# Kernel tuning notes

Hardware: AMD Instinct MI355X
Metric: run time of the kernel (lower is better)

Reference implementation:

```python
import jax, jax.numpy as jnp
import numpy as np

N = 100000   # nodes
E = 1600000  # edges
IN, H, OUT = 128, 128, 64
EPS = 1e-5   # BatchNorm1d eps


def setup_inputs() -> dict:
    key = jax.random.key(0)
    ks = jax.random.split(key, 6)
    glorot = lambda k, i, o: jax.random.normal(k, (i, o), jnp.float32) / np.float32(np.sqrt(i))
    return {
        "x": jax.random.normal(ks[0], (N, IN), jnp.float32),
        "edge_index": jax.random.randint(ks[1], (2, E), 0, N, dtype=jnp.int32),
        "W1": glorot(ks[2], IN, H),
        "b1": jnp.zeros((H,), jnp.float32),
        "g1": jnp.ones((H,), jnp.float32),
        "be1": jnp.zeros((H,), jnp.float32),
        "W2": glorot(ks[3], H, H),
        "b2": jnp.zeros((H,), jnp.float32),
        "g2": jnp.ones((H,), jnp.float32),
        "be2": jnp.zeros((H,), jnp.float32),
        "W3": glorot(ks[4], H, OUT),
        "b3": jnp.zeros((OUT,), jnp.float32),
    }


def _gcn_conv(x, W, b, src, dst, dinv):
    # PyG GCNConv: h = x @ W (no linear bias); symmetric-normalized scatter-add
    # over edges with implicit self-loops; then additive bias.
    h = x @ W                                           # [N, F]
    coef = (dinv[src] * dinv[dst])[:, None]             # [E, 1]
    agg = jax.ops.segment_sum(h[src] * coef, dst, num_segments=N)
    agg = agg + h * (dinv * dinv)[:, None]              # self-loop term
    return agg + b


def _bn(x, g, b):
    # BatchNorm1d, training-mode batch statistics (biased variance).
    m = jnp.mean(x, axis=0)
    v = jnp.mean(jnp.square(x - m), axis=0)
    return (x - m) * jax.lax.rsqrt(v + EPS) * g + b


def reference(x, edge_index, W1, b1, g1, be1, W2, b2, g2, be2, W3, b3):
    src, dst = edge_index[0], edge_index[1]
    # degree with self-loops (edge weights = 1)
    deg = jax.ops.segment_sum(jnp.ones((E,), jnp.float32), dst, num_segments=N) + 1.0
    dinv = jax.lax.rsqrt(deg)

    x1 = jax.nn.relu(_bn(_gcn_conv(x, W1, b1, src, dst, dinv), g1, be1))
    x2 = jax.nn.relu(_bn(_gcn_conv(x1, W2, b2, src, dst, dinv), g2, be2))
    x2 = x2 + x1                                        # skip connection
    return _gcn_conv(x2, W3, b3, src, dst, dinv)
```

## Files before the change

kernel.cpp:

```cpp
#include <hip/hip_runtime.h>

#define BN_EPS 1e-5f

typedef unsigned short ushort_t;
typedef __attribute__((ext_vector_type(8))) short bf16x8;
typedef __attribute__((ext_vector_type(16))) float f32x16;

__device__ __forceinline__ ushort_t bf16rne(float f) {
    unsigned int u = __float_as_uint(f);
    unsigned int r = (u + 0x7FFFu + ((u >> 16) & 1u)) >> 16;
    return (ushort_t)r;
}
__device__ __forceinline__ unsigned int pack2(float a, float b) {
    return (unsigned int)bf16rne(a) | ((unsigned int)bf16rne(b) << 16);
}
__device__ __forceinline__ void cvt2(unsigned int u, float& lo, float& hi) {
    lo = __uint_as_float(u << 16);
    hi = __uint_as_float(u & 0xFFFF0000u);
}
__device__ __forceinline__ bf16x8 as_bf16x8(uint4 u) {
    union { uint4 u; bf16x8 v; } c; c.u = u; return c.v;
}


#define BIN_CHUNK 4096

__global__ __launch_bounds__(256) void k_binhist(const int* __restrict__ dst, int E, int NB,
                                                 int* __restrict__ bucket_counts) {
    __shared__ int hist[512];
    for (int i = threadIdx.x; i < NB; i += 256) hist[i] = 0;
    __syncthreads();
    int base = blockIdx.x * BIN_CHUNK;
    int end = min(E, base + BIN_CHUNK);
    for (int e = base + threadIdx.x; e < end; e += 256)
        atomicAdd(&hist[dst[e] >> 8], 1);
    __syncthreads();
    for (int i = threadIdx.x; i < NB; i += 256)
        if (hist[i]) atomicAdd(&bucket_counts[i], hist[i]);
}

__global__ void k_bucketscan(const int* __restrict__ bucket_counts, int NB, int N, int E,
                             int* __restrict__ bucket_base, int* __restrict__ bucket_cursor,
                             int* __restrict__ rowptr) {
    __shared__ int sh[512];
    int t = threadIdx.x;
    int v = (t < NB) ? bucket_counts[t] : 0;
    sh[t] = v;
    __syncthreads();
    for (int off = 1; off < 512; off <<= 1) {
        int x = (t >= off) ? sh[t - off] : 0;
        __syncthreads();
        sh[t] += x;
        __syncthreads();
    }
    if (t < NB) {
        int b = sh[t] - v;
        bucket_base[t] = b;
        bucket_cursor[t] = b;
    }
    if (t == 0) { bucket_base[NB] = E; rowptr[N] = E; }
}

__global__ __launch_bounds__(256) void k_bin(const int* __restrict__ src,
                                             const int* __restrict__ dst, int E, int NB,
                                             int* __restrict__ bucket_cursor,
                                             unsigned int* __restrict__ binned) {
    __shared__ int hist[512];
    __shared__ int cur[512];
    for (int i = threadIdx.x; i < NB; i += 256) hist[i] = 0;
    __syncthreads();
    int base = blockIdx.x * BIN_CHUNK;
    int end = min(E, base + BIN_CHUNK);
    for (int e = base + threadIdx.x; e < end; e += 256)
        atomicAdd(&hist[dst[e] >> 8], 1);
    __syncthreads();
    for (int i = threadIdx.x; i < NB; i += 256)
        cur[i] = hist[i] ? atomicAdd(&bucket_cursor[i], hist[i]) : 0;
    __syncthreads();
    for (int e = base + threadIdx.x; e < end; e += 256) {
        int d = dst[e];
        int pos = atomicAdd(&cur[d >> 8], 1);
        binned[pos] = (unsigned int)src[e] | ((unsigned int)(d & 255) << 24);
    }
}

__global__ __launch_bounds__(256) void k_bucket(const unsigned int* __restrict__ binned,
                                                const int* __restrict__ bucket_base, int N,
                                                int* __restrict__ rowptr,
                                                float* __restrict__ dinv,
                                                int* __restrict__ csr_src) {
    __shared__ int cnt[256];
    __shared__ int sh[256];
    __shared__ int cur[256];
    int b = blockIdx.x;
    int t = threadIdx.x;
    int node0 = b << 8;
    int lo = bucket_base[b], hi = bucket_base[b + 1];
    cnt[t] = 0;
    __syncthreads();
    for (int p = lo + t; p < hi; p += 256)
        atomicAdd(&cnt[binned[p] >> 24], 1);
    __syncthreads();
    int v = cnt[t];
    sh[t] = v;
    __syncthreads();
    for (int off = 1; off < 256; off <<= 1) {
        int y = (t >= off) ? sh[t - off] : 0;
        __syncthreads();
        sh[t] += y;
        __syncthreads();
    }
    int gbase = lo + (sh[t] - v);
    int node = node0 + t;
    if (node < N) {
        rowptr[node] = gbase;
        dinv[node] = rsqrtf((float)v + 1.0f);
    }
    cur[t] = gbase;
    __syncthreads();
    for (int p = lo + t; p < hi; p += 256) {
        unsigned int pr = binned[p];
        int pos = atomicAdd(&cur[pr >> 24], 1);
        csr_src[pos] = (int)(pr & 0xFFFFFFu);
    }
}


__global__ __launch_bounds__(256) void k_statreduce(const float* __restrict__ partial,
                                                    int nblk, float* __restrict__ sp256) {
    int t = threadIdx.x;
    float acc = 0.f;
    for (int r = blockIdx.x; r < nblk; r += gridDim.x)
        acc += partial[(size_t)r * 256 + t];
    atomicAdd(&sp256[t], acc);
}

__global__ void k_bnparam(const float* __restrict__ sp256, const float* __restrict__ g,
                          const float* __restrict__ be, float* __restrict__ scale,
                          float* __restrict__ shift, float invN) {
    int j = threadIdx.x;
    int cg = j >> 3, klo = j & 7;
    float s = sp256[(klo << 4) | cg];
    float q = sp256[((klo + 8) << 4) | cg];
    float m = s * invN;
    float var = q * invN - m * m;
    float r = rsqrtf(var + BN_EPS);
    float sc = g[j] * r;
    scale[j] = sc;
    shift[j] = be[j] - m * sc;
}


__global__ void k_wprep(const float* __restrict__ W, ushort_t* __restrict__ BT, int M) {
    int col = blockIdx.x;
    int k = threadIdx.x;
    BT[col * 128 + k] = bf16rne(W[k * M + col]);
}

__global__ __launch_bounds__(256) void k_xcvt(const float* __restrict__ X,
                                              ushort_t* __restrict__ Xb, int total8) {
    int i = blockIdx.x * 256 + threadIdx.x;
    if (i >= total8) return;
    float4 a = ((const float4*)X)[2 * i];
    float4 b = ((const float4*)X)[2 * i + 1];
    uint4 po;
    po.x = pack2(a.x, a.y); po.y = pack2(a.z, a.w);
    po.z = pack2(b.x, b.y); po.w = pack2(b.z, b.w);
    ((uint4*)Xb)[i] = po;
}

template<bool ADDSKIP>
__global__ __launch_bounds__(256) void k_bntrans(const ushort_t* __restrict__ Ain,
                                                 const float* __restrict__ scale,
                                                 const float* __restrict__ shift,
                                                 const ushort_t* __restrict__ skip,
                                                 ushort_t* __restrict__ Outb, int N) {
    int i = blockIdx.x * 256 + threadIdx.x;
    if (i >= N * 16) return;
    int j0 = (i & 15) * 8;
    uint4 raw = ((const uint4*)Ain)[i];
    float v[8];
    cvt2(raw.x, v[0], v[1]); cvt2(raw.y, v[2], v[3]);
    cvt2(raw.z, v[4], v[5]); cvt2(raw.w, v[6], v[7]);
    float4 sc0 = *(const float4*)&scale[j0];
    float4 sc1 = *(const float4*)&scale[j0 + 4];
    float4 sh0 = *(const float4*)&shift[j0];
    float4 sh1 = *(const float4*)&shift[j0 + 4];
    v[0] = fmaxf(v[0] * sc0.x + sh0.x, 0.f);
    v[1] = fmaxf(v[1] * sc0.y + sh0.y, 0.f);
    v[2] = fmaxf(v[2] * sc0.z + sh0.z, 0.f);
    v[3] = fmaxf(v[3] * sc0.w + sh0.w, 0.f);
    v[4] = fmaxf(v[4] * sc1.x + sh1.x, 0.f);
    v[5] = fmaxf(v[5] * sc1.y + sh1.y, 0.f);
    v[6] = fmaxf(v[6] * sc1.z + sh1.z, 0.f);
    v[7] = fmaxf(v[7] * sc1.w + sh1.w, 0.f);
    if constexpr (ADDSKIP) {
        uint4 s4 = ((const uint4*)skip)[i];
        float lo, hi;
        cvt2(s4.x, lo, hi); v[0] += lo; v[1] += hi;
        cvt2(s4.y, lo, hi); v[2] += lo; v[3] += hi;
        cvt2(s4.z, lo, hi); v[4] += lo; v[5] += hi;
        cvt2(s4.w, lo, hi); v[6] += lo; v[7] += hi;
    }
    uint4 po;
    po.x = pack2(v[0], v[1]); po.y = pack2(v[2], v[3]);
    po.z = pack2(v[4], v[5]); po.w = pack2(v[6], v[7]);
    ((uint4*)Outb)[i] = po;
}


template<int M>
__global__ __launch_bounds__(256) void k_mgemm(const ushort_t* __restrict__ A,
                                               const ushort_t* __restrict__ BT,
                                               ushort_t* __restrict__ Out, int N) {
    constexpr int CT = M / 32;
    int wid = threadIdx.x >> 6;
    int lane = threadIdx.x & 63;
    int l31 = lane & 31;
    int khalf = (lane >> 5) * 8;
    int rowbase = blockIdx.x * 128 + wid * 32;
    int arow = rowbase + l31;

    f32x16 acc[CT] = {};

#pragma unroll
    for (int ks = 0; ks < 8; ++ks) {
        bf16x8 af = {};
        if (arow < N)
            af = as_bf16x8(*(const uint4*)&A[(size_t)arow * 128 + ks * 16 + khalf]);
#pragma unroll
        for (int ct = 0; ct < CT; ++ct) {
            int bcol = ct * 32 + l31;
            bf16x8 bfr = as_bf16x8(*(const uint4*)&BT[(size_t)bcol * 128 + ks * 16 + khalf]);
            acc[ct] = __builtin_amdgcn_mfma_f32_32x32x16_bf16(af, bfr, acc[ct], 0, 0, 0);
        }
    }

#pragma unroll
    for (int ct = 0; ct < CT; ++ct) {
        int col = ct * 32 + l31;
#pragma unroll
        for (int q = 0; q < 16; ++q) {
            int row = rowbase + (q & 3) + 8 * (q >> 2) + 4 * (lane >> 5);
            if (row < N)
                Out[(size_t)row * M + col] = bf16rne(acc[ct][q]);
        }
    }
}


template<int M, bool STATS, bool BF16OUT>
__global__ __launch_bounds__(256) void k_agg(const ushort_t* __restrict__ Hm,
                      const int* __restrict__ rowptr,
                      const int* __restrict__ csr_src, const float* __restrict__ dinv,
                      const float* __restrict__ bias, void* __restrict__ Out, int N,
                      float* __restrict__ partial) {
    constexpr int TPN = M / 8;
    constexpr int NPB = 256 / TPN;
    int li = threadIdx.x / TPN;
    int lane = threadIdx.x % TPN;
    int i = blockIdx.x * NPB + li;
    bool valid = (i < N);
    int j0 = lane * 8;

    float o[8] = {0.f, 0.f, 0.f, 0.f, 0.f, 0.f, 0.f, 0.f};

    if (valid) {
        int p = rowptr[i], p1 = rowptr[i + 1];
        for (; p + 3 < p1; p += 4) {
            int s0 = csr_src[p + 0];
            int s1 = csr_src[p + 1];
            int s2 = csr_src[p + 2];
            int s3 = csr_src[p + 3];
            float c0 = dinv[s0], c1 = dinv[s1], c2 = dinv[s2], c3 = dinv[s3];
            uint4 g0 = *(const uint4*)&Hm[(size_t)s0 * M + j0];
            uint4 g1 = *(const uint4*)&Hm[(size_t)s1 * M + j0];
            uint4 g2 = *(const uint4*)&Hm[(size_t)s2 * M + j0];
            uint4 g3 = *(const uint4*)&Hm[(size_t)s3 * M + j0];
            float lo, hi;
            cvt2(g0.x, lo, hi); o[0] += lo * c0; o[1] += hi * c0;
            cvt2(g0.y, lo, hi); o[2] += lo * c0; o[3] += hi * c0;
            cvt2(g0.z, lo, hi); o[4] += lo * c0; o[5] += hi * c0;
            cvt2(g0.w, lo, hi); o[6] += lo * c0; o[7] += hi * c0;
            cvt2(g1.x, lo, hi); o[0] += lo * c1; o[1] += hi * c1;
            cvt2(g1.y, lo, hi); o[2] += lo * c1; o[3] += hi * c1;
            cvt2(g1.z, lo, hi); o[4] += lo * c1; o[5] += hi * c1;
            cvt2(g1.w, lo, hi); o[6] += lo * c1; o[7] += hi * c1;
            cvt2(g2.x, lo, hi); o[0] += lo * c2; o[1] += hi * c2;
            cvt2(g2.y, lo, hi); o[2] += lo * c2; o[3] += hi * c2;
            cvt2(g2.z, lo, hi); o[4] += lo * c2; o[5] += hi * c2;
            cvt2(g2.w, lo, hi); o[6] += lo * c2; o[7] += hi * c2;
            cvt2(g3.x, lo, hi); o[0] += lo * c3; o[1] += hi * c3;
            cvt2(g3.y, lo, hi); o[2] += lo * c3; o[3] += hi * c3;
            cvt2(g3.z, lo, hi); o[4] += lo * c3; o[5] += hi * c3;
            cvt2(g3.w, lo, hi); o[6] += lo * c3; o[7] += hi * c3;
        }
        for (; p < p1; ++p) {
            int s = csr_src[p];
            float cf = dinv[s];
            uint4 g = *(const uint4*)&Hm[(size_t)s * M + j0];
            float lo, hi;
            cvt2(g.x, lo, hi); o[0] += lo * cf; o[1] += hi * cf;
            cvt2(g.y, lo, hi); o[2] += lo * cf; o[3] += hi * cf;
            cvt2(g.z, lo, hi); o[4] += lo * cf; o[5] += hi * cf;
            cvt2(g.w, lo, hi); o[6] += lo * cf; o[7] += hi * cf;
        }

        float di = dinv[i];
        uint4 hs = *(const uint4*)&Hm[(size_t)i * M + j0];
        float lo, hi;
        cvt2(hs.x, lo, hi); o[0] += lo * di; o[1] += hi * di;
        cvt2(hs.y, lo, hi); o[2] += lo * di; o[3] += hi * di;
        cvt2(hs.z, lo, hi); o[4] += lo * di; o[5] += hi * di;
        cvt2(hs.w, lo, hi); o[6] += lo * di; o[7] += hi * di;

        float4 bv0 = *(const float4*)&bias[j0];
        float4 bv1 = *(const float4*)&bias[j0 + 4];
        o[0] = o[0] * di + bv0.x; o[1] = o[1] * di + bv0.y;
        o[2] = o[2] * di + bv0.z; o[3] = o[3] * di + bv0.w;
        o[4] = o[4] * di + bv1.x; o[5] = o[5] * di + bv1.y;
        o[6] = o[6] * di + bv1.z; o[7] = o[7] * di + bv1.w;
    }

    if constexpr (STATS) {
        float st[16];
#pragma unroll
        for (int k = 0; k < 8; ++k) { st[k] = o[k]; st[8 + k] = o[k] * o[k]; }
#pragma unroll
        for (int k = 0; k < 16; ++k) {
            st[k] += __shfl_xor(st[k], 16);
            st[k] += __shfl_xor(st[k], 32);
        }
        __shared__ float red[4][16][16];
        int wv = threadIdx.x >> 6;
        int ln = threadIdx.x & 63;
        if (ln < 16) {
#pragma unroll
            for (int k = 0; k < 16; ++k) red[wv][ln][k] = st[k];
        }
        __syncthreads();
        {
            int t = threadIdx.x;
            int cg = t & 15, k = t >> 4;
            float s = red[0][cg][k] + red[1][cg][k] + red[2][cg][k] + red[3][cg][k];
            partial[(size_t)blockIdx.x * 256 + t] = s;
        }
    }

    if constexpr (BF16OUT) {
        if (valid) {
            uint4 po;
            po.x = pack2(o[0], o[1]); po.y = pack2(o[2], o[3]);
            po.z = pack2(o[4], o[5]); po.w = pack2(o[6], o[7]);
            *(uint4*)&((ushort_t*)Out)[(size_t)i * M + j0] = po;
        }
    } else {
        __shared__ float outs[NPB][M + 4];
#pragma unroll
        for (int cc = 0; cc < 8; ++cc) outs[li][lane * 8 + cc] = o[cc];
        __syncthreads();
        float* Of = (float*)Out;
        int i0 = blockIdx.x * NPB;
        constexpr int Q = M / 4;
        for (int f = threadIdx.x; f < NPB * Q; f += 256) {
            int node = f / Q;
            int q = f % Q;
            if (i0 + node < N)
                *(float4*)&Of[(size_t)(i0 + node) * M + q * 4] = *(float4*)&outs[node][q * 4];
        }
    }
}


extern "C" void kernel_launch(void* const* d_in, const int* in_sizes, int n_in,
                              void* d_out, int out_size, void* d_ws, size_t ws_size,
                              hipStream_t stream) {
    const float* x   = (const float*)d_in[0];
    const int*   ei  = (const int*)d_in[1];
    const float* W1  = (const float*)d_in[2];
    const float* b1  = (const float*)d_in[3];
    const float* g1  = (const float*)d_in[4];
    const float* be1 = (const float*)d_in[5];
    const float* W2  = (const float*)d_in[6];
    const float* b2  = (const float*)d_in[7];
    const float* g2  = (const float*)d_in[8];
    const float* be2 = (const float*)d_in[9];
    const float* W3  = (const float*)d_in[10];
    const float* b3  = (const float*)d_in[11];

    int N = in_sizes[0] / 128;
    int E = in_sizes[1] / 2;
    const int* srcp = ei;
    const int* dstp = ei + E;
    int NB = (N + 255) >> 8;

    char* ws = (char*)d_ws;
    size_t off = 0;
    auto alloc = [&](size_t bytes) {
        void* p = ws + off;
        off += (bytes + 255) & ~(size_t)255;
        return p;
    };

    int nblk128 = (N + 15) / 16;

    int*   rowptr   = (int*)alloc(((size_t)N + 1) * 4);
    int*   csr_src  = (int*)alloc((size_t)E * 4);
    float* dinv     = (float*)alloc((size_t)N * 4);
    int*   bucket_counts = (int*)alloc(512 * 4);
    int*   bucket_base   = (int*)alloc(513 * 4);
    int*   bucket_cursor = (int*)alloc(512 * 4);
    float* partialA = (float*)alloc((size_t)nblk128 * 256 * 4);
    float* partialB = (float*)alloc((size_t)nblk128 * 256 * 4);
    float* sp256A   = (float*)alloc(256 * 4);
    float* sp256B   = (float*)alloc(256 * 4);
    float* scale1   = (float*)alloc(128 * 4);
    float* shift1   = (float*)alloc(128 * 4);
    float* scale2   = (float*)alloc(128 * 4);
    float* shift2   = (float*)alloc(128 * 4);
    ushort_t* BT1   = (ushort_t*)alloc(128 * 128 * 2);
    ushort_t* BT2   = (ushort_t*)alloc(128 * 128 * 2);
    ushort_t* BT3   = (ushort_t*)alloc(64 * 128 * 2);
    ushort_t* xbf   = (ushort_t*)alloc((size_t)N * 128 * 2);
    ushort_t* hbuf  = (ushort_t*)alloc((size_t)N * 128 * 2);
    ushort_t* x1bf  = (ushort_t*)alloc((size_t)N * 128 * 2);
    ushort_t* x2bf  = (ushort_t*)alloc((size_t)N * 128 * 2);
    ushort_t* abuf1 = (ushort_t*)alloc((size_t)N * 128 * 2);
    ushort_t* abuf2 = (ushort_t*)alloc((size_t)N * 128 * 2);
    unsigned int* binned = (unsigned int*)abuf1;

    float invN = 1.0f / (float)N;
    int nbE = (E + BIN_CHUNK - 1) / BIN_CHUNK;
    int gemmBlocks = (N + 127) / 128;
    int ncvt8 = N * 16;

    hipMemsetAsync(bucket_counts, 0, 512 * 4, stream);
    k_binhist<<<nbE, 256, 0, stream>>>(dstp, E, NB, bucket_counts);
    k_bucketscan<<<1, 512, 0, stream>>>(bucket_counts, NB, N, E,
                                        bucket_base, bucket_cursor, rowptr);
    k_bin<<<nbE, 256, 0, stream>>>(srcp, dstp, E, NB, bucket_cursor, binned);
    k_bucket<<<NB, 256, 0, stream>>>(binned, bucket_base, N, rowptr, dinv, csr_src);
    hipMemsetAsync(sp256A, 0, 256 * 4, stream);
    hipMemsetAsync(sp256B, 0, 256 * 4, stream);

    k_wprep<<<128, 128, 0, stream>>>(W1, BT1, 128);
    k_wprep<<<128, 128, 0, stream>>>(W2, BT2, 128);
    k_wprep<<<64, 128, 0, stream>>>(W3, BT3, 64);
    k_xcvt<<<(ncvt8 + 255) / 256, 256, 0, stream>>>(x, xbf, ncvt8);

    k_mgemm<128><<<gemmBlocks, 256, 0, stream>>>(xbf, BT1, hbuf, N);
    k_agg<128, true, true><<<nblk128, 256, 0, stream>>>(hbuf, rowptr, csr_src, dinv,
                                                        b1, abuf1, N, partialA);
    k_statreduce<<<256, 256, 0, stream>>>(partialA, nblk128, sp256A);
    k_bnparam<<<1, 128, 0, stream>>>(sp256A, g1, be1, scale1, shift1, invN);

    k_bntrans<false><<<(ncvt8 + 255) / 256, 256, 0, stream>>>(abuf1, scale1, shift1,
                                                              nullptr, x1bf, N);
    k_mgemm<128><<<gemmBlocks, 256, 0, stream>>>(x1bf, BT2, hbuf, N);
    k_agg<128, true, true><<<nblk128, 256, 0, stream>>>(hbuf, rowptr, csr_src, dinv,
                                                        b2, abuf2, N, partialB);
    k_statreduce<<<256, 256, 0, stream>>>(partialB, nblk128, sp256B);
    k_bnparam<<<1, 128, 0, stream>>>(sp256B, g2, be2, scale2, shift2, invN);

    k_bntrans<true><<<(ncvt8 + 255) / 256, 256, 0, stream>>>(abuf2, scale2, shift2,
                                                             x1bf, x2bf, N);
    k_mgemm<64><<<gemmBlocks, 256, 0, stream>>>(x2bf, BT3, hbuf, N);
    k_agg<64, false, false><<<(N + 31) / 32, 256, 0, stream>>>(hbuf, rowptr, csr_src, dinv,
                                                               b3, d_out, N, nullptr);
}
```

Before: 374.9 us.

## Store node features in column-sliced planar layout for cache-local gather aggregation

Feature matrices become column-panel planar: 8 slices of 16 (or 8) columns, each laid out contiguously over all nodes. Each aggregation block now handles one slice for a group of nodes, so a block's random gathers stay within a smaller panel that fits better in L2/MALL. The GEMM, conversion, BN-transform and stats kernels are rewritten to read and write this layout. In exchange, CSR indices and dinv are re-read once per slice (8x index traffic), and the GEMM writes become strided.

Measured after the change: 622.5 us. +66.1%, slower.

```diff
diff --git a/kernel.cpp b/kernel.cpp
--- a/kernel.cpp
+++ b/kernel.cpp
@@ -21,6 +21,7 @@
 __device__ __forceinline__ bf16x8 as_bf16x8(uint4 u) {
     union { uint4 u; bf16x8 v; } c; c.u = u; return c.v;
 }
+
 
 
 #define BIN_CHUNK 4096
@@ -127,23 +128,24 @@
 
 
 __global__ __launch_bounds__(256) void k_statreduce(const float* __restrict__ partial,
-                                                    int nblk, float* __restrict__ sp256) {
+                                                    int ngroups, float* __restrict__ sp) {
     int t = threadIdx.x;
+    int tau = t >> 7;
+    int j = t & 127;
+    int slice = j >> 4;
+    int idx = tau * 16 + (j & 15);
     float acc = 0.f;
-    for (int r = blockIdx.x; r < nblk; r += gridDim.x)
-        acc += partial[(size_t)r * 256 + t];
-    atomicAdd(&sp256[t], acc);
-}
-
-__global__ void k_bnparam(const float* __restrict__ sp256, const float* __restrict__ g,
+    for (int r = blockIdx.x; r < ngroups; r += gridDim.x)
+        acc += partial[(size_t)(r * 8 + slice) * 32 + idx];
+    atomicAdd(&sp[tau * 128 + j], acc);
+}
+
+__global__ void k_bnparam(const float* __restrict__ sp, const float* __restrict__ g,
                           const float* __restrict__ be, float* __restrict__ scale,
                           float* __restrict__ shift, float invN) {
     int j = threadIdx.x;
-    int cg = j >> 3, klo = j & 7;
-    float s = sp256[(klo << 4) | cg];
-    float q = sp256[((klo + 8) << 4) | cg];
-    float m = s * invN;
-    float var = q * invN - m * m;
+    float m = sp[j] * invN;
+    float var = sp[128 + j] * invN - m * m;
     float r = rsqrtf(var + BN_EPS);
     float sc = g[j] * r;
     scale[j] = sc;
@@ -158,15 +160,20 @@
 }
 
 __global__ __launch_bounds__(256) void k_xcvt(const float* __restrict__ X,
-                                              ushort_t* __restrict__ Xb, int total8) {
-    int i = blockIdx.x * 256 + threadIdx.x;
-    if (i >= total8) return;
-    float4 a = ((const float4*)X)[2 * i];
-    float4 b = ((const float4*)X)[2 * i + 1];
+                                              ushort_t* __restrict__ Xp, int N) {
+    int u = blockIdx.x * 256 + threadIdx.x;
+    int per = N * 2;
+    if (u >= per * 8) return;
+    int p = u / per;
+    int w = u - p * per;
+    int row = w >> 1, half = w & 1;
+    int j0 = p * 16 + half * 8;
+    float4 a = *(const float4*)&X[(size_t)row * 128 + j0];
+    float4 b = *(const float4*)&X[(size_t)row * 128 + j0 + 4];
     uint4 po;
     po.x = pack2(a.x, a.y); po.y = pack2(a.z, a.w);
     po.z = pack2(b.x, b.y); po.w = pack2(b.z, b.w);
-    ((uint4*)Xb)[i] = po;
+    ((uint4*)Xp)[u] = po;
 }
 
 template<bool ADDSKIP>
@@ -175,10 +182,14 @@
                                                  const float* __restrict__ shift,
                                                  const ushort_t* __restrict__ skip,
                                                  ushort_t* __restrict__ Outb, int N) {
-    int i = blockIdx.x * 256 + threadIdx.x;
-    if (i >= N * 16) return;
-    int j0 = (i & 15) * 8;
-    uint4 raw = ((const uint4*)Ain)[i];
+    int u = blockIdx.x * 256 + threadIdx.x;
+    int per = N * 2;
+    if (u >= per * 8) return;
+    int p = u / per;
+    int w = u - p * per;
+    int half = w & 1;
+    int j0 = p * 16 + half * 8;
+    uint4 raw = ((const uint4*)Ain)[u];
     float v[8];
     cvt2(raw.x, v[0], v[1]); cvt2(raw.y, v[2], v[3]);
     cvt2(raw.z, v[4], v[5]); cvt2(raw.w, v[6], v[7]);
@@ -195,7 +206,7 @@
     v[6] = fmaxf(v[6] * sc1.z + sh1.z, 0.f);
     v[7] = fmaxf(v[7] * sc1.w + sh1.w, 0.f);
     if constexpr (ADDSKIP) {
-        uint4 s4 = ((const uint4*)skip)[i];
+        uint4 s4 = ((const uint4*)skip)[u];
         float lo, hi;
         cvt2(s4.x, lo, hi); v[0] += lo; v[1] += hi;
         cvt2(s4.y, lo, hi); v[2] += lo; v[3] += hi;
@@ -205,7 +216,7 @@
     uint4 po;
     po.x = pack2(v[0], v[1]); po.y = pack2(v[2], v[3]);
     po.z = pack2(v[4], v[5]); po.w = pack2(v[6], v[7]);
-    ((uint4*)Outb)[i] = po;
+    ((uint4*)Outb)[u] = po;
 }
 
 
@@ -214,12 +225,15 @@
                                                const ushort_t* __restrict__ BT,
                                                ushort_t* __restrict__ Out, int N) {
     constexpr int CT = M / 32;
+    constexpr int PC = (M == 128) ? 16 : 8;
     int wid = threadIdx.x >> 6;
     int lane = threadIdx.x & 63;
     int l31 = lane & 31;
     int khalf = (lane >> 5) * 8;
     int rowbase = blockIdx.x * 128 + wid * 32;
     int arow = rowbase + l31;
+    size_t N16 = (size_t)N * 16;
+    size_t NPC = (size_t)N * PC;
 
     f32x16 acc[CT] = {};
 
@@ -227,7 +241,7 @@
     for (int ks = 0; ks < 8; ++ks) {
         bf16x8 af = {};
         if (arow < N)
-            af = as_bf16x8(*(const uint4*)&A[(size_t)arow * 128 + ks * 16 + khalf]);
+            af = as_bf16x8(*(const uint4*)&A[ks * N16 + (size_t)arow * 16 + khalf]);
 #pragma unroll
         for (int ct = 0; ct < CT; ++ct) {
             int bcol = ct * 32 + l31;
@@ -239,29 +253,32 @@
 #pragma unroll
     for (int ct = 0; ct < CT; ++ct) {
         int col = ct * 32 + l31;
+        size_t pb = (size_t)(col / PC) * NPC + (col % PC);
 #pragma unroll
         for (int q = 0; q < 16; ++q) {
             int row = rowbase + (q & 3) + 8 * (q >> 2) + 4 * (lane >> 5);
             if (row < N)
-                Out[(size_t)row * M + col] = bf16rne(acc[ct][q]);
-        }
-    }
-}
-
-
-template<int M, bool STATS, bool BF16OUT>
-__global__ __launch_bounds__(256) void k_agg(const ushort_t* __restrict__ Hm,
+                Out[pb + (size_t)row * PC] = bf16rne(acc[ct][q]);
+        }
+    }
+}
+
+
+template<bool STATS>
+__global__ __launch_bounds__(256) void k_aggs128(const ushort_t* __restrict__ Hm,
                       const int* __restrict__ rowptr,
                       const int* __restrict__ csr_src, const float* __restrict__ dinv,
-                      const float* __restrict__ bias, void* __restrict__ Out, int N,
+                      const float* __restrict__ bias, ushort_t* __restrict__ Out, int N,
                       float* __restrict__ partial) {
-    constexpr int TPN = M / 8;
-    constexpr int NPB = 256 / TPN;
-    int li = threadIdx.x / TPN;
-    int lane = threadIdx.x % TPN;
-    int i = blockIdx.x * NPB + li;
+    int slice = blockIdx.x & 7;
+    int grp = blockIdx.x >> 3;
+    int li = threadIdx.x >> 1;
+    int ln = threadIdx.x & 1;
+    int i = grp * 128 + li;
     bool valid = (i < N);
-    int j0 = lane * 8;
+    size_t pbase = (size_t)slice * N * 16;
+    int po = ln * 8;
+    int j0 = slice * 16 + po;
 
     float o[8] = {0.f, 0.f, 0.f, 0.f, 0.f, 0.f, 0.f, 0.f};
 
@@ -273,10 +290,10 @@
             int s2 = csr_src[p + 2];
             int s3 = csr_src[p + 3];
             float c0 = dinv[s0], c1 = dinv[s1], c2 = dinv[s2], c3 = dinv[s3];
-            uint4 g0 = *(const uint4*)&Hm[(size_t)s0 * M + j0];
-            uint4 g1 = *(const uint4*)&Hm[(size_t)s1 * M + j0];
-            uint4 g2 = *(const uint4*)&Hm[(size_t)s2 * M + j0];
-            uint4 g3 = *(const uint4*)&Hm[(size_t)s3 * M + j0];
+            uint4 g0 = *(const uint4*)&Hm[pbase + (size_t)s0 * 16 + po];
+            uint4 g1 = *(const uint4*)&Hm[pbase + (size_t)s1 * 16 + po];
+            uint4 g2 = *(const uint4*)&Hm[pbase + (size_t)s2 * 16 + po];
+            uint4 g3 = *(const uint4*)&Hm[pbase + (size_t)s3 * 16 + po];
             float lo, hi;
             cvt2(g0.x, lo, hi); o[0] += lo * c0; o[1] += hi * c0;
             cvt2(g0.y, lo, hi); o[2] += lo * c0; o[3] += hi * c0;
@@ -298,7 +315,7 @@
         for (; p < p1; ++p) {
             int s = csr_src[p];
             float cf = dinv[s];
-            uint4 g = *(const uint4*)&Hm[(size_t)s * M + j0];
+            uint4 g = *(const uint4*)&Hm[pbase + (size_t)s * 16 + po];
             float lo, hi;
             cvt2(g.x, lo, hi); o[0] += lo * cf; o[1] += hi * cf;
             cvt2(g.y, lo, hi); o[2] += lo * cf; o[3] += hi * cf;
@@ -307,7 +324,7 @@
         }
 
         float di = dinv[i];
-        uint4 hs = *(const uint4*)&Hm[(size_t)i * M + j0];
+        uint4 hs = *(const uint4*)&Hm[pbase + (size_t)i * 16 + po];
         float lo, hi;
         cvt2(hs.x, lo, hi); o[0] += lo * di; o[1] += hi * di;
         cvt2(hs.y, lo, hi); o[2] += lo * di; o[3] += hi * di;
@@ -328,47 +345,109 @@
         for (int k = 0; k < 8; ++k) { st[k] = o[k]; st[8 + k] = o[k] * o[k]; }
 #pragma unroll
         for (int k = 0; k < 16; ++k) {
+            st[k] += __shfl_xor(st[k], 2);
+            st[k] += __shfl_xor(st[k], 4);
+            st[k] += __shfl_xor(st[k], 8);
             st[k] += __shfl_xor(st[k], 16);
             st[k] += __shfl_xor(st[k], 32);
         }
-        __shared__ float red[4][16][16];
+        __shared__ float red[4][2][16];
         int wv = threadIdx.x >> 6;
-        int ln = threadIdx.x & 63;
-        if (ln < 16) {
-#pragma unroll
-            for (int k = 0; k < 16; ++k) red[wv][ln][k] = st[k];
+        int l64 = threadIdx.x & 63;
+        if (l64 < 2) {
+#pragma unroll
+            for (int k = 0; k < 16; ++k) red[wv][l64][k] = st[k];
         }
         __syncthreads();
-        {
+        if (threadIdx.x < 32) {
             int t = threadIdx.x;
-            int cg = t & 15, k = t >> 4;
-            float s = red[0][cg][k] + red[1][cg][k] + red[2][cg][k] + red[3][cg][k];
-            partial[(size_t)blockIdx.x * 256 + t] = s;
-        }
-    }
-
-    if constexpr (BF16OUT) {
-        if (valid) {
-            uint4 po;
-            po.x = pack2(o[0], o[1]); po.y = pack2(o[2], o[3]);
-            po.z = pack2(o[4], o[5]); po.w = pack2(o[6], o[7]);
-            *(uint4*)&((ushort_t*)Out)[(size_t)i * M + j0] = po;
-        }
-    } else {
-        __shared__ float outs[NPB][M + 4];
-#pragma unroll
-        for (int cc = 0; cc < 8; ++cc) outs[li][lane * 8 + cc] = o[cc];
-        __syncthreads();
-        float* Of = (float*)Out;
-        int i0 = blockIdx.x * NPB;
-        constexpr int Q = M / 4;
-        for (int f = threadIdx.x; f < NPB * Q; f += 256) {
-            int node = f / Q;
-            int q = f % Q;
-            if (i0 + node < N)
-                *(float4*)&Of[(size_t)(i0 + node) * M + q * 4] = *(float4*)&outs[node][q * 4];
-        }
-    }
+            int lnn = t >> 4, k = t & 15;
+            float s = red[0][lnn][k] + red[1][lnn][k] + red[2][lnn][k] + red[3][lnn][k];
+            int stat = k >> 3;
+            int c = lnn * 8 + (k & 7);
+            partial[(size_t)blockIdx.x * 32 + stat * 16 + c] = s;
+        }
+    }
+
+    if (valid) {
+        uint4 po4;
+        po4.x = pack2(o[0], o[1]); po4.y = pack2(o[2], o[3]);
+        po4.z = pack2(o[4], o[5]); po4.w = pack2(o[6], o[7]);
+        *(uint4*)&Out[pbase + (size_t)i * 16 + po] = po4;
+    }
+}
+
+
+__global__ __launch_bounds__(256) void k_aggs64(const ushort_t* __restrict__ Hm,
+                      const int* __restrict__ rowptr,
+                      const int* __restrict__ csr_src, const float* __restrict__ dinv,
+                      const float* __restrict__ bias, float* __restrict__ Out, int N) {
+    int slice = blockIdx.x & 7;
+    int grp = blockIdx.x >> 3;
+    int i = grp * 256 + threadIdx.x;
+    if (i >= N) return;
+    size_t pbase = (size_t)slice * N * 8;
+    int j0 = slice * 8;
+
+    float o[8] = {0.f, 0.f, 0.f, 0.f, 0.f, 0.f, 0.f, 0.f};
+
+    int p = rowptr[i], p1 = rowptr[i + 1];
+    for (; p + 3 < p1; p += 4) {
+        int s0 = csr_src[p + 0];
+        int s1 = csr_src[p + 1];
+        int s2 = csr_src[p + 2];
+        int s3 = csr_src[p + 3];
+        float c0 = dinv[s0], c1 = dinv[s1], c2 = dinv[s2], c3 = dinv[s3];
+        uint4 g0 = *(const uint4*)&Hm[pbase + (size_t)s0 * 8];
+        uint4 g1 = *(const uint4*)&Hm[pbase + (size_t)s1 * 8];
+        uint4 g2 = *(const uint4*)&Hm[pbase + (size_t)s2 * 8];
+        uint4 g3 = *(const uint4*)&Hm[pbase + (size_t)s3 * 8];
+        float lo, hi;
+        cvt2(g0.x, lo, hi); o[0] += lo * c0; o[1] += hi * c0;
+        cvt2(g0.y, lo, hi); o[2] += lo * c0; o[3] += hi * c0;
+        cvt2(g0.z, lo, hi); o[4] += lo * c0; o[5] += hi * c0;
+        cvt2(g0.w, lo, hi); o[6] += lo * c0; o[7] += hi * c0;
+        cvt2(g1.x, lo, hi); o[0] += lo * c1; o[1] += hi * c1;
+        cvt2(g1.y, lo, hi); o[2] += lo * c1; o[3] += hi * c1;
+        cvt2(g1.z, lo, hi); o[4] += lo * c1; o[5] += hi * c1;
+        cvt2(g1.w, lo, hi); o[6] += lo * c1; o[7] += hi * c1;
+        cvt2(g2.x, lo, hi); o[0] += lo * c2; o[1] += hi * c2;
+        cvt2(g2.y, lo, hi); o[2] += lo * c2; o[3] += hi * c2;
+        cvt2(g2.z, lo, hi); o[4] += lo * c2; o[5] += hi * c2;
+        cvt2(g2.w, lo, hi); o[6] += lo * c2; o[7] += hi * c2;
+        cvt2(g3.x, lo, hi); o[0] += lo * c3; o[1] += hi * c3;
+        cvt2(g3.y, lo, hi); o[2] += lo * c3; o[3] += hi * c3;
+        cvt2(g3.z, lo, hi); o[4] += lo * c3; o[5] += hi * c3;
+        cvt2(g3.w, lo, hi); o[6] += lo * c3; o[7] += hi * c3;
+    }
+    for (; p < p1; ++p) {
+        int s = csr_src[p];
+        float cf = dinv[s];
+        uint4 g = *(const uint4*)&Hm[pbase + (size_t)s * 8];
+        float lo, hi;
+        cvt2(g.x, lo, hi); o[0] += lo * cf; o[1] += hi * cf;
+        cvt2(g.y, lo, hi); o[2] += lo * cf; o[3] += hi * cf;
+        cvt2(g.z, lo, hi); o[4] += lo * cf; o[5] += hi * cf;
+        cvt2(g.w, lo, hi); o[6] += lo * cf; o[7] += hi * cf;
+    }
+
+    float di = dinv[i];
+    uint4 hs = *(const uint4*)&Hm[pbase + (size_t)i * 8];
+    float lo, hi;
+    cvt2(hs.x, lo, hi); o[0] += lo * di; o[1] += hi * di;
+    cvt2(hs.y, lo, hi); o[2] += lo * di; o[3] += hi * di;
+    cvt2(hs.z, lo, hi); o[4] += lo * di; o[5] += hi * di;
+    cvt2(hs.w, lo, hi); o[6] += lo * di; o[7] += hi * di;
+
+    float4 bv0 = *(const float4*)&bias[j0];
+    float4 bv1 = *(const float4*)&bias[j0 + 4];
+    float4 o0, o1;
+    o0.x = o[0] * di + bv0.x; o0.y = o[1] * di + bv0.y;
+    o0.z = o[2] * di + bv0.z; o0.w = o[3] * di + bv0.w;
+    o1.x = o[4] * di + bv1.x; o1.y = o[5] * di + bv1.y;
+    o1.z = o[6] * di + bv1.z; o1.w = o[7] * di + bv1.w;
+    *(float4*)&Out[(size_t)i * 64 + j0] = o0;
+    *(float4*)&Out[(size_t)i * 64 + j0 + 4] = o1;
 }
 
 
@@ -402,7 +481,7 @@
         return p;
     };
 
-    int nblk128 = (N + 15) / 16;
+    int ngroups128 = (N + 127) / 128;
 
     int*   rowptr   = (int*)alloc(((size_t)N + 1) * 4);
     int*   csr_src  = (int*)alloc((size_t)E * 4);
@@ -410,10 +489,10 @@
     int*   bucket_counts = (int*)alloc(512 * 4);
     int*   bucket_base   = (int*)alloc(513 * 4);
     int*   bucket_cursor = (int*)alloc(512 * 4);
-    float* partialA = (float*)alloc((size_t)nblk128 * 256 * 4);
-    float* partialB = (float*)alloc((size_t)nblk128 * 256 * 4);
-    float* sp256A   = (float*)alloc(256 * 4);
-    float* sp256B   = (float*)alloc(256 * 4);
+    float* partialA = (float*)alloc((size_t)ngroups128 * 8 * 32 * 4);
+    float* partialB = (float*)alloc((size_t)ngroups128 * 8 * 32 * 4);
+    float* spA      = (float*)alloc(256 * 4);
+    float* spB      = (float*)alloc(256 * 4);
     float* scale1   = (float*)alloc(128 * 4);
     float* shift1   = (float*)alloc(128 * 4);
     float* scale2   = (float*)alloc(128 * 4);
@@ -432,7 +511,7 @@
     float invN = 1.0f / (float)N;
     int nbE = (E + BIN_CHUNK - 1) / BIN_CHUNK;
     int gemmBlocks = (N + 127) / 128;
-    int ncvt8 = N * 16;
+    int ncvt = N * 16;
 
     hipMemsetAsync(bucket_counts, 0, 512 * 4, stream);
     k_binhist<<<nbE, 256, 0, stream>>>(dstp, E, NB, bucket_counts);
@@ -440,31 +519,32 @@
                                         bucket_base, bucket_cursor, rowptr);
     k_bin<<<nbE, 256, 0, stream>>>(srcp, dstp, E, NB, bucket_cursor, binned);
     k_bucket<<<NB, 256, 0, stream>>>(binned, bucket_base, N, rowptr, dinv, csr_src);
-    hipMemsetAsync(sp256A, 0, 256 * 4, stream);
-    hipMemsetAsync(sp256B, 0, 256 * 4, stream);
+    hipMemsetAsync(spA, 0, 256 * 4, stream);
+    hipMemsetAsync(spB, 0, 256 * 4, stream);
 
     k_wprep<<<128, 128, 0, stream>>>(W1, BT1, 128);
     k_wprep<<<128, 128, 0, stream>>>(W2, BT2, 128);
     k_wprep<<<64, 128, 0, stream>>>(W3, BT3, 64);
-    k_xcvt<<<(ncvt8 + 255) / 256, 256, 0, stream>>>(x, xbf, ncvt8);
+    k_xcvt<<<(ncvt + 255) / 256, 256, 0, stream>>>(x, xbf, N);
 
     k_mgemm<128><<<gemmBlocks, 256, 0, stream>>>(xbf, BT1, hbuf, N);
-    k_agg<128, true, true><<<nblk128, 256, 0, stream>>>(hbuf, rowptr, csr_src, dinv,
+    k_aggs128<true><<<ngroups128 * 8, 256, 0, stream>>>(hbuf, rowptr, csr_src, dinv,
                                                         b1, abuf1, N, partialA);
-    k_statreduce<<<256, 256, 0, stream>>>(partialA, nblk128, sp256A);
-    k_bnparam<<<1, 128, 0, stream>>>(sp256A, g1, be1, scale1, shift1, invN);
-
-    k_bntrans<false><<<(ncvt8 + 255) / 256, 256, 0, stream>>>(abuf1, scale1, shift1,
-                                                              nullptr, x1bf, N);
+    k_statreduce<<<256, 256, 0, stream>>>(partialA, ngroups128, spA);
+    k_bnparam<<<1, 128, 0, stream>>>(spA, g1, be1, scale1, shift1, invN);
+
+    k_bntrans<false><<<(ncvt + 255) / 256, 256, 0, stream>>>(abuf1, scale1, shift1,
+                                                             nullptr, x1bf, N);
     k_mgemm<128><<<gemmBlocks, 256, 0, stream>>>(x1bf, BT2, hbuf, N);
-    k_agg<128, true, true><<<nblk128, 256, 0, stream>>>(hbuf, rowptr, csr_src, dinv,
+    k_aggs128<true><<<ngroups128 * 8, 256, 0, stream>>>(hbuf, rowptr, csr_src, dinv,
                                                         b2, abuf2, N, partialB);
-    k_statreduce<<<256, 256, 0, stream>>>(partialB, nblk128, sp256B);
-    k_bnparam<<<1, 128, 0, stream>>>(sp256B, g2, be2, scale2, shift2, invN);
-
-    k_bntrans<true><<<(ncvt8 + 255) / 256, 256, 0, stream>>>(abuf2, scale2, shift2,
-                                                             x1bf, x2bf, N);
+    k_statreduce<<<256, 256, 0, stream>>>(partialB, ngroups128, spB);
+    k_bnparam<<<1, 128, 0, stream>>>(spB, g2, be2, scale2, shift2, invN);
+
+    k_bntrans<true><<<(ncvt + 255) / 256, 256, 0, stream>>>(abuf2, scale2, shift2,
+                                                            x1bf, x2bf, N);
     k_mgemm<64><<<gemmBlocks, 256, 0, stream>>>(x2bf, BT3, hbuf, N);
-    k_agg<64, false, false><<<(N + 31) / 32, 256, 0, stream>>>(hbuf, rowptr, csr_src, dinv,
-                                                               b3, d_out, N, nullptr);
-}
+    int ngroups64 = (N + 255) / 256;
+    k_aggs64<<<ngroups64 * 8, 256, 0, stream>>>(hbuf, rowptr, csr_src, dinv,
+                                                b3, (float*)d_out, N);
+}
```
